# Optimization experiments

Hardware: AMD Instinct MI355X
Metric: run time of the kernel (lower is better)

## Reference

```python
import jax, jax.numpy as jnp
import numpy as np
from itertools import combinations

DIM = 3
METRIC = np.array([1.0, 1.0, 1.0], dtype=np.float32)
KERNEL_SIZE = 7
C_IN, C_OUT = 32, 32
HIDDEN = 64
NUM_LAYERS = 4
N_GRID = KERNEL_SIZE ** DIM


def _build_cayley(dim, metric):
    blades = [()] + [c for r in range(1, dim + 1) for c in combinations(range(dim), r)]
    idx = {b: i for i, b in enumerate(blades)}
    n = len(blades)
    C = np.zeros((n, n, n), dtype=np.float32)
    for i, a in enumerate(blades):
        for j, b in enumerate(blades):
            arr = list(a) + list(b)
            sign = 1.0
            changed = True
            while changed:
                changed = False
                t = 0
                while t < len(arr) - 1:
                    if arr[t] == arr[t + 1]:
                        sign *= metric[arr[t]]
                        del arr[t:t + 2]
                        changed = True
                        break
                    if arr[t] > arr[t + 1]:
                        arr[t], arr[t + 1] = arr[t + 1], arr[t]
                        sign = -sign
                        changed = True
                    t += 1
            C[i, j, idx[tuple(arr)]] = sign
    grades = np.array([len(b) for b in blades])
    return C, grades

_C_LRO, GRADES = _build_cayley(DIM, METRIC)
CAYLEY = np.transpose(_C_LRO, (0, 2, 1))  # [left, out, right] (CEGNN convention)
N_BLADES = CAYLEY.shape[0]
N_GRADES = DIM + 1

# nonzero grade-triple paths of the Cayley tensor and blade-level path-id lookup
_gp = np.zeros((N_GRADES,) * 3, dtype=bool)
for a in range(N_GRADES):
    for b in range(N_GRADES):
        for c in range(N_GRADES):
            _gp[a, b, c] = np.any(CAYLEY[np.ix_(GRADES == a, GRADES == b, GRADES == c)] != 0)
PATHS = np.argwhere(_gp)
P = len(PATHS)
assert P == 20  # product_paths_sum for Cl(3,0)
_pid = -np.ones((N_GRADES,) * 3, dtype=np.int64)
for p, (a, b, c) in enumerate(PATHS):
    _pid[a, b, c] = p
BLADE_PID = _pid[GRADES[:, None, None], GRADES[None, :, None], GRADES[None, None, :]]
BLADE_PID = np.where(BLADE_PID < 0, P, BLADE_PID)  # P -> zero slot

# centered relative-position grid, (N, 1, dim)
_ax = np.arange(KERNEL_SIZE, dtype=np.float32) - (KERNEL_SIZE - 1) / 2.0
_grid = np.stack(np.meshgrid(*([_ax] * DIM), indexing='ij'), axis=-1).reshape(-1, DIM)
REL_POS = jnp.asarray(_grid[:, None, :])
CAYLEY_J = jnp.asarray(CAYLEY)
GRADE_ONEHOT = jnp.asarray((GRADES[:, None] == np.arange(N_GRADES)[None, :]).astype(np.float32))
FACTOR = 1.0 / np.sqrt(float(KERNEL_SIZE ** DIM))
BLADES_OF = {g: np.where(GRADES == g)[0] for g in range(N_GRADES)}


def embed_grade(x, g):
    out = jnp.zeros(x.shape[:-1] + (N_BLADES,), x.dtype)
    return out.at[..., BLADES_OF[g]].set(x)


def expand_paths(w):
    # (..., P) grade-path weights -> (..., B, B, B) blade-level weights
    wz = jnp.concatenate([w, jnp.zeros(w.shape[:-1] + (1,), w.dtype)], axis=-1)
    return wz[..., BLADE_PID]


def mv_linear(x, W, b):
    # grade-wise equivariant channel mixing; x: (N,Ci,B), W: (G,Co,Ci), bias on scalar blade
    y = jnp.einsum('boi,nib->nob', W[GRADES], x)
    return y.at[:, :, 0].add(b)


def mv_silu(x, a, b):
    # gate each grade by sigmoid of its (learned-scaled) squared norm
    qg = jnp.einsum('ncb,bg->ncg', x * x, GRADE_ONEHOT)
    gate = jax.nn.sigmoid(a * qg + b)
    return x * gate[:, :, GRADES]


def gp_layer(x, w):
    # fully-connected steerable geometric product; x: (N,C,B), w: (Co,C,P)
    wc = expand_paths(w) * CAYLEY_J  # (Co, C, B, B, B)
    y = jnp.einsum('nik,oikjm,nim->noj', x, wc, x)
    return y / np.sqrt(float(x.shape[1]))


def setup_inputs() -> dict:
    key = jax.random.key(0)
    ks = jax.random.split(key, 8)
    G, B, H, Pn = N_GRADES, N_BLADES, HIDDEN, P
    rn = lambda k, s, sc: jax.random.normal(k, s, dtype=jnp.float32) * sc
    ci1 = C_IN + 1
    return {
        'condition': rn(ks[0], (C_IN, B), 1.0),
        'rel_pos_sigma': jnp.ones((1, 1, 1), jnp.float32),
        'cayley_w': rn(ks[1], (C_OUT, C_IN, Pn), 1.0 / np.sqrt(C_IN)),
        'lin0_W': rn(ks[2], (G, H, ci1), 1.0 / np.sqrt(ci1)),
        'lin0_b': jnp.zeros((H,), jnp.float32),
        'act0_a': rn(ks[3], (H, G), 0.2),
        'act0_b': jnp.zeros((H, G), jnp.float32),
        'gps_w': rn(ks[4], (NUM_LAYERS, H, H, Pn), 0.5 / np.sqrt(H)),
        'lins_W': rn(ks[5], (NUM_LAYERS - 1, G, H, H), 1.0 / np.sqrt(H)),
        'lins_b': jnp.zeros((NUM_LAYERS - 1, H), jnp.float32),
        'acts_a': rn(ks[6], (NUM_LAYERS - 1, H, G), 0.2),
        'acts_b': jnp.zeros((NUM_LAYERS - 1, H, G), jnp.float32),
        'out_W': rn(ks[7], (G, C_OUT * C_IN, H), 1.0 / np.sqrt(H)),
        'out_b': jnp.zeros((C_OUT * C_IN,), jnp.float32),
        'shell_sigma': jnp.ones((1, C_OUT, C_IN, B), jnp.float32),
    }


def reference(condition, rel_pos_sigma, cayley_w, lin0_W, lin0_b, act0_a, act0_b,
              gps_w, lins_W, lins_b, acts_a, acts_b, out_W, out_b, shell_sigma):
    metric = jnp.asarray(METRIC)
    q = jnp.sum(metric * REL_POS * REL_POS, axis=-1, keepdims=True)  # (N,1,1)
    scalar = jnp.exp(-q / (2.0 * rel_pos_sigma ** 2))
    x = embed_grade(scalar, 0) + embed_grade(REL_POS, 1)  # (N,1,B)
    cond = jnp.broadcast_to(condition[None], (N_GRID,) + condition.shape)
    x = jnp.concatenate([x, cond], axis=1)  # (N, c_in+1, B)
    # kernel network: CEGNN blocks [MVLinear -> MVSiLU -> steerable geometric product]
    h = gp_layer(mv_silu(mv_linear(x, lin0_W, lin0_b), act0_a, act0_b), gps_w[0])
    for l in range(NUM_LAYERS - 1):
        h = gp_layer(mv_silu(mv_linear(h, lins_W[l], lins_b[l]), acts_a[l], acts_b[l]), gps_w[l + 1])
    k = mv_linear(h, out_W, out_b).reshape(N_GRID, C_OUT, C_IN, N_BLADES)
    # per-(c_out,c_in,blade) scalar radial shell
    shell = jnp.exp(-q.reshape(N_GRID, 1, 1, 1) / (shell_sigma ** 2))
    k = k * shell * FACTOR
    # kernel head: sparse weighted-Cayley contraction
    wc = expand_paths(cayley_w) * CAYLEY_J  # (c_out, c_in, B, B, B)
    K = jnp.einsum('noik,oiklm->olimn', k, wc)
    return K.reshape(C_OUT * N_BLADES, C_IN * N_BLADES, KERNEL_SIZE, KERNEL_SIZE, KERNEL_SIZE)
```

## Files before the change

### kernel.cpp

```cpp
#include <hip/hip_runtime.h>
#include <math.h>

#define NB 8
#define NGRID 343
#define HID 64
#define NPATH 20

struct Tab {
  int prod_idx[8][8];
  int prod_sgn[8][8];
  int pid[4][4][4];
  int grade[8];
  int kk_idx[8][8];
  int kk_sgn[8][8];
};

constexpr Tab make_tab() {
  Tab t{};
  int mask[8]  = {0,1,2,4,3,5,6,7};
  int idxof[8] = {0,1,2,4,3,5,6,7};
  for (int k = 0; k < 8; ++k) {
    int g = 0;
    for (int b = 0; b < 3; ++b) g += (mask[k] >> b) & 1;
    t.grade[k] = g;
  }
  for (int k = 0; k < 8; ++k)
    for (int m = 0; m < 8; ++m) {
      int A = mask[k], B = mask[m];
      t.prod_idx[k][m] = idxof[A ^ B];
      int c = 0;
      for (int i = 0; i < 3; ++i)
        if ((B >> i) & 1)
          for (int j = i + 1; j < 3; ++j)
            if ((A >> j) & 1) c++;
      t.prod_sgn[k][m] = (c & 1) ? -1 : 1;
    }
  int pc = 0;
  for (int a = 0; a < 4; ++a)
    for (int b = 0; b < 4; ++b)
      for (int c = 0; c < 4; ++c) {
        bool ok = false;
        for (int k = 0; k < 8; ++k)
          for (int m = 0; m < 8; ++m)
            if (t.grade[k] == a && t.grade[m] == c &&
                t.grade[t.prod_idx[k][m]] == b)
              ok = true;
        t.pid[a][b][c] = ok ? pc++ : NPATH;
      }
  for (int l = 0; l < 8; ++l)
    for (int m = 0; m < 8; ++m)
      for (int k = 0; k < 8; ++k)
        if (t.prod_idx[k][m] == l) {
          t.kk_idx[l][m] = k;
          t.kk_sgn[l][m] = t.prod_sgn[k][m];
        }
  return t;
}
constexpr Tab TB = make_tab();

#define OFF_LIN0T 0
#define OFF_LINST 8448
#define OFF_GPST  57600
#define OFF_OUTWT 385280
#define OFF_KWS   647424

__global__ void ccs_prep_kernel(const float* __restrict__ lin0_W,
                                const float* __restrict__ lins_W,
                                const float* __restrict__ gps_w,
                                const float* __restrict__ out_W,
                                float* __restrict__ ws) {
  const int TOT = 8448 + 49152 + 327680 + 262144;
  for (int d = blockIdx.x * blockDim.x + threadIdx.x; d < TOT;
       d += gridDim.x * blockDim.x) {
    float v;
    if (d < 8448) {
      int idx = d;
      int hh = idx & 63, ch = (idx >> 6) % 33, g = (idx >> 6) / 33;
      v = lin0_W[(g * 64 + hh) * 33 + ch];
    } else if (d < 8448 + 49152) {
      int idx = d - OFF_LINST;
      int hh = idx & 63, i = (idx >> 6) & 63, g = (idx >> 12) & 3, l = idx >> 14;
      v = lins_W[((l * 4 + g) * 64 + hh) * 64 + i];
    } else if (d < 8448 + 49152 + 327680) {
      int idx = d - OFF_GPST;
      int o = idx & 63, p = (idx >> 6) % 20, i = ((idx >> 6) / 20) & 63,
          l = idx / 81920;
      v = gps_w[((l * 64 + o) * 64 + i) * 20 + p];
    } else {
      int idx = d - OFF_OUTWT;
      int oc = idx & 1023, i = (idx >> 10) & 63, g = idx >> 16;
      v = out_W[(g * 1024 + oc) * 64 + i];
    }
    ws[d] = v;
  }
}

__launch_bounds__(512)
__global__ void ccs_net_kernel(const float* __restrict__ condition,
                               const float* __restrict__ rel_pos_sigma,
                               const float* __restrict__ lin0_b,
                               const float* __restrict__ act0_a,
                               const float* __restrict__ act0_b,
                               const float* __restrict__ lins_b,
                               const float* __restrict__ acts_a,
                               const float* __restrict__ acts_b,
                               const float* __restrict__ out_b,
                               const float* __restrict__ shell_sigma,
                               const float* __restrict__ ws,
                               float* __restrict__ kws) {
  const float* lin0t = ws + OFF_LIN0T;
  const float* linst = ws + OFF_LINST;
  const float* gpst  = ws + OFF_GPST;
  const float* outwt = ws + OFF_OUTWT;

  __shared__ float xb[33 * 8];
  __shared__ float x0r[2][8];
  __shared__ __align__(16) float F0[2 * 512];
  __shared__ __align__(16) float F1[2 * 512];
  __shared__ float part[2 * 8 * 8 * 64];

  const int tid = threadIdx.x;
  const int n0 = blockIdx.x * 2;
  const int n1 = n0 + 1;

  const float sig = rel_pos_sigma[0];

  float qq[2];
  {
    int iz = n0 % 7, iy = (n0 / 7) % 7, ix = n0 / 49;
    float px = (float)ix - 3.f, py = (float)iy - 3.f, pz = (float)iz - 3.f;
    qq[0] = px * px + py * py + pz * pz;
  }
  {
    int nc = (n1 < NGRID) ? n1 : (NGRID - 1);
    int iz = nc % 7, iy = (nc / 7) % 7, ix = nc / 49;
    float px = (float)ix - 3.f, py = (float)iy - 3.f, pz = (float)iz - 3.f;
    qq[1] = px * px + py * py + pz * pz;
  }

  for (int t = tid; t < 264; t += 512) {
    int ch = t >> 3, b = t & 7;
    xb[t] = (ch == 0) ? 0.f : condition[(ch - 1) * 8 + b];
  }
  if (tid < 16) {
    int pt = tid >> 3, b = tid & 7;
    int nc = n0 + pt;
    if (nc >= NGRID) nc = NGRID - 1;
    int iz = nc % 7, iy = (nc / 7) % 7, ix = nc / 49;
    float px = (float)ix - 3.f, py = (float)iy - 3.f, pz = (float)iz - 3.f;
    float q = px * px + py * py + pz * pz;
    float scal = expf(-q / (2.f * sig * sig));
    x0r[pt][b] =
        (b == 0) ? scal : (b == 1) ? px : (b == 2) ? py : (b == 3) ? pz : 0.f;
  }
  __syncthreads();

  const int b8 = tid & 7;
  const int hh = (tid >> 3) & 63;
  const int gb = TB.grade[b8];

  {
    const float* wrow = lin0t + gb * 33 * 64 + hh;
    float w0 = wrow[0];
    float a0 = w0 * x0r[0][b8];
    float a1 = w0 * x0r[1][b8];
    if (b8 == 0) {
      float bb = lin0_b[hh];
      a0 += bb;
      a1 += bb;
    }
    #pragma unroll
    for (int ch = 1; ch < 33; ++ch) {
      float w = wrow[ch * 64];
      float xv = xb[ch * 8 + b8];
      a0 = fmaf(w, xv, a0);
      a1 = fmaf(w, xv, a1);
    }
    F0[hh * 8 + b8] = a0;
    F0[512 + hh * 8 + b8] = a1;
  }
  __syncthreads();

  auto silu = [&](const float* src, float* dst, const float* aa,
                  const float* bb) {
    int s0 = (gb == 0) ? 0 : (gb == 1) ? 1 : (gb == 2) ? 4 : 7;
    int cnt = (gb == 0 || gb == 3) ? 1 : 3;
    float A = aa[hh * 4 + gb], B = bb[hh * 4 + gb];
    #pragma unroll
    for (int pt = 0; pt < 2; ++pt) {
      float qg = 0.f;
      for (int u = 0; u < cnt; ++u) {
        float v = src[pt * 512 + hh * 8 + s0 + u];
        qg = fmaf(v, v, qg);
      }
      float z = fmaf(A, qg, B);
      float gate = 1.f / (1.f + expf(-z));
      dst[pt * 512 + hh * 8 + b8] = src[pt * 512 + hh * 8 + b8] * gate;
    }
  };

  auto lin = [&](const float* src, float* dst, const float* wt,
                 const float* bias) {
    const float* wrow = wt + gb * 64 * 64 + hh;
    float a0 = 0.f, a1 = 0.f;
    if (b8 == 0) {
      float bb = bias[hh];
      a0 = bb;
      a1 = bb;
    }
    #pragma unroll
    for (int i = 0; i < 64; ++i) {
      float w = wrow[i * 64];
      a0 = fmaf(w, src[i * 8 + b8], a0);
      a1 = fmaf(w, src[512 + i * 8 + b8], a1);
    }
    dst[hh * 8 + b8] = a0;
    dst[512 + hh * 8 + b8] = a1;
  };

  auto gp = [&](const float* src, float* dst, const float* wl) {
    const int o = tid & 63;
    const int isub = tid >> 6;
    float fa[8], fb[8];
    #pragma unroll
    for (int j = 0; j < 8; ++j) {
      fa[j] = 0.f;
      fb[j] = 0.f;
    }
    for (int it = 0; it < 8; ++it) {
      int i = isub * 8 + it;
      float4 va0 = *(const float4*)(src + i * 8);
      float4 va1 = *(const float4*)(src + i * 8 + 4);
      float4 vb0 = *(const float4*)(src + 512 + i * 8);
      float4 vb1 = *(const float4*)(src + 512 + i * 8 + 4);
      float xA[8] = {va0.x, va0.y, va0.z, va0.w, va1.x, va1.y, va1.z, va1.w};
      float xB[8] = {vb0.x, vb0.y, vb0.z, vb0.w, vb1.x, vb1.y, vb1.z, vb1.w};
      const float* wb = wl + i * 20 * 64 + o;
      float wp[20];
      #pragma unroll
      for (int p = 0; p < 20; ++p) wp[p] = wb[p * 64];
      #pragma unroll
      for (int k = 0; k < 8; ++k) {
        #pragma unroll
        for (int m = 0; m < 8; ++m) {
          const int j = TB.prod_idx[k][m];
          const int p = TB.pid[TB.grade[k]][TB.grade[j]][TB.grade[m]];
          if (TB.prod_sgn[k][m] > 0) {
            fa[j] = fmaf(xA[k] * xA[m], wp[p], fa[j]);
            fb[j] = fmaf(xB[k] * xB[m], wp[p], fb[j]);
          } else {
            fa[j] = fmaf(-xA[k] * xA[m], wp[p], fa[j]);
            fb[j] = fmaf(-xB[k] * xB[m], wp[p], fb[j]);
          }
        }
      }
    }
    #pragma unroll
    for (int j = 0; j < 8; ++j) {
      part[isub * 512 + j * 64 + o] = fa[j];
      part[4096 + isub * 512 + j * 64 + o] = fb[j];
    }
    __syncthreads();
    #pragma unroll
    for (int r = 0; r < 2; ++r) {
      int item = tid + r * 512;
      int oo = item & 63;
      int j = (item >> 6) & 7;
      int pt = item >> 9;
      const float* pp = part + pt * 4096 + j * 64 + oo;
      float s = pp[0] + pp[512] + pp[1024] + pp[1536] + pp[2048] + pp[2560] +
                pp[3072] + pp[3584];
      dst[pt * 512 + oo * 8 + j] = s * 0.125f;
    }
    __syncthreads();
  };

  silu(F0, F1, act0_a, act0_b);
  __syncthreads();
  gp(F1, F0, gpst + 0);

  float* f = F0;
  float* g_ = F1;
  for (int l = 0; l < 3; ++l) {
    lin(f, g_, linst + l * 16384, lins_b + l * 64);
    __syncthreads();
    silu(g_, f, acts_a + l * 256, acts_b + l * 256);
    __syncthreads();
    gp(f, g_, gpst + (l + 1) * 81920);
    float* t = f; f = g_; g_ = t;
  }

  const float FACTOR = 1.0f / sqrtf(343.0f);
  #pragma unroll
  for (int r = 0; r < 2; ++r) {
    int oc = tid + r * 512;
    float acc[2][8];
    #pragma unroll
    for (int pt = 0; pt < 2; ++pt)
      #pragma unroll
      for (int b = 0; b < 8; ++b) acc[pt][b] = 0.f;
    {
      float bb = out_b[oc];
      acc[0][0] = bb;
      acc[1][0] = bb;
    }
    #pragma unroll 4
    for (int i = 0; i < 64; ++i) {
      float w0 = outwt[(0 * 64 + i) * 1024 + oc];
      float w1 = outwt[(1 * 64 + i) * 1024 + oc];
      float w2 = outwt[(2 * 64 + i) * 1024 + oc];
      float w3 = outwt[(3 * 64 + i) * 1024 + oc];
      #pragma unroll
      for (int pt = 0; pt < 2; ++pt) {
        float h[8];
        *(float4*)h = *(const float4*)(f + pt * 512 + i * 8);
        *(float4*)(h + 4) = *(const float4*)(f + pt * 512 + i * 8 + 4);
        acc[pt][0] = fmaf(w0, h[0], acc[pt][0]);
        acc[pt][1] = fmaf(w1, h[1], acc[pt][1]);
        acc[pt][2] = fmaf(w1, h[2], acc[pt][2]);
        acc[pt][3] = fmaf(w1, h[3], acc[pt][3]);
        acc[pt][4] = fmaf(w2, h[4], acc[pt][4]);
        acc[pt][5] = fmaf(w2, h[5], acc[pt][5]);
        acc[pt][6] = fmaf(w2, h[6], acc[pt][6]);
        acc[pt][7] = fmaf(w3, h[7], acc[pt][7]);
      }
    }
    float sh[8];
    *(float4*)sh = *(const float4*)(shell_sigma + oc * 8);
    *(float4*)(sh + 4) = *(const float4*)(shell_sigma + oc * 8 + 4);
    #pragma unroll
    for (int pt = 0; pt < 2; ++pt) {
      int n = n0 + pt;
      if (n < NGRID) {
        float q = qq[pt];
        float out8[8];
        #pragma unroll
        for (int b = 0; b < 8; ++b)
          out8[b] = acc[pt][b] * expf(-q / (sh[b] * sh[b])) * FACTOR;
        float4* dstp = (float4*)(kws + ((size_t)oc * 343 + n) * 8);
        dstp[0] = make_float4(out8[0], out8[1], out8[2], out8[3]);
        dstp[1] = make_float4(out8[4], out8[5], out8[6], out8[7]);
      }
    }
  }
}

__launch_bounds__(256)
__global__ void ccs_expand_kernel(const float* __restrict__ cayley_w,
                                  const float* __restrict__ kws,
                                  float* __restrict__ out) {
  const int oi = blockIdx.x;
  const int tid = threadIdx.x;
  __shared__ float kT[8][344];

  const float4* src = (const float4*)(kws + (size_t)oi * 343 * 8);
  for (int t = tid; t < 686; t += 256) {
    float4 v = src[t];
    int n = t >> 1, b = (t & 1) * 4;
    kT[b][n] = v.x;
    kT[b + 1][n] = v.y;
    kT[b + 2][n] = v.z;
    kT[b + 3][n] = v.w;
  }
  float cw[20];
  #pragma unroll
  for (int p = 0; p < 20; ++p) cw[p] = cayley_w[oi * 20 + p];
  __syncthreads();

  const int o = oi >> 5, i = oi & 31;
  #pragma unroll
  for (int l = 0; l < 8; ++l) {
    #pragma unroll
    for (int m = 0; m < 8; ++m) {
      const int kk = TB.kk_idx[l][m];
      const int p = TB.pid[TB.grade[kk]][TB.grade[l]][TB.grade[m]];
      float c = (TB.kk_sgn[l][m] < 0) ? -cw[p] : cw[p];
      float* dst = out + ((size_t)((o * 8 + l) * 256 + i * 8 + m)) * 343;
      dst[tid] = kT[kk][tid] * c;
      if (tid < 343 - 256) dst[tid + 256] = kT[kk][tid + 256] * c;
    }
  }
}

extern "C" void kernel_launch(void* const* d_in, const int* in_sizes, int n_in,
                              void* d_out, int out_size, void* d_ws,
                              size_t ws_size, hipStream_t stream) {
  const float* condition     = (const float*)d_in[0];
  const float* rel_pos_sigma = (const float*)d_in[1];
  const float* cayley_w      = (const float*)d_in[2];
  const float* lin0_W        = (const float*)d_in[3];
  const float* lin0_b        = (const float*)d_in[4];
  const float* act0_a        = (const float*)d_in[5];
  const float* act0_b        = (const float*)d_in[6];
  const float* gps_w         = (const float*)d_in[7];
  const float* lins_W        = (const float*)d_in[8];
  const float* lins_b        = (const float*)d_in[9];
  const float* acts_a        = (const float*)d_in[10];
  const float* acts_b        = (const float*)d_in[11];
  const float* out_W         = (const float*)d_in[12];
  const float* out_b         = (const float*)d_in[13];
  const float* shell_sigma   = (const float*)d_in[14];

  float* ws = (float*)d_ws;
  float* kws = ws + OFF_KWS;
  float* out = (float*)d_out;

  ccs_prep_kernel<<<dim3(640), dim3(256), 0, stream>>>(lin0_W, lins_W, gps_w,
                                                       out_W, ws);
  ccs_net_kernel<<<dim3((NGRID + 1) / 2), dim3(512), 0, stream>>>(
      condition, rel_pos_sigma, lin0_b, act0_a, act0_b, lins_b, acts_a, acts_b,
      out_b, shell_sigma, ws, kws);
  ccs_expand_kernel<<<dim3(1024), dim3(256), 0, stream>>>(cayley_w, kws, out);
}
```

Measured before the change: 226.2 us.

## Double-buffer geometric-product weights into LDS with async global_load_lds prefetch

The geometric-product layer now streams its per-layer weights into a two-slot LDS buffer using asynchronous global-to-LDS loads, issued two chunks ahead. Explicit vmcnt waits replace the per-iteration global loads. The input-channel mapping is changed so each wave consumes only the chunk slice it loaded itself, which avoids block barriers. The goal is to hide global-memory latency behind the FMA-heavy product loop. In exchange it adds about 80 KB of LDS per block and relies on hand-counted vmcnt values, which is fragile if the compiler emits other vector-memory operations.

```diff
diff --git a/kernel.cpp b/kernel.cpp
--- a/kernel.cpp
+++ b/kernel.cpp
@@ -95,6 +95,12 @@
   }
 }
 
+__device__ __forceinline__ void glds16(const float* g, float* l) {
+  __builtin_amdgcn_global_load_lds(
+      (const __attribute__((address_space(1))) unsigned int*)g,
+      (__attribute__((address_space(3))) unsigned int*)l, 16, 0, 0);
+}
+
 __launch_bounds__(512)
 __global__ void ccs_net_kernel(const float* __restrict__ condition,
                                const float* __restrict__ rel_pos_sigma,
@@ -118,6 +124,7 @@
   __shared__ __align__(16) float F0[2 * 512];
   __shared__ __align__(16) float F1[2 * 512];
   __shared__ float part[2 * 8 * 8 * 64];
+  __shared__ __align__(16) float wch[2][10240];
 
   const int tid = threadIdx.x;
   const int n0 = blockIdx.x * 2;
@@ -220,25 +227,43 @@
 
   auto gp = [&](const float* src, float* dst, const float* wl) {
     const int o = tid & 63;
-    const int isub = tid >> 6;
+    const int w = tid >> 6;
+    const int w5 = w * 5;
+    const int ln4 = (tid & 63) * 4;
     float fa[8], fb[8];
     #pragma unroll
     for (int j = 0; j < 8; ++j) {
       fa[j] = 0.f;
       fb[j] = 0.f;
     }
-    for (int it = 0; it < 8; ++it) {
-      int i = isub * 8 + it;
+    auto issue = [&](int c) {
+      const float* gbch = wl + c * 10240;
+      float* lbch = &wch[c & 1][0];
+      #pragma unroll
+      for (int u = 0; u < 5; ++u) {
+        int t = w5 + u;
+        glds16(gbch + t * 256 + ln4, lbch + t * 256);
+      }
+    };
+    issue(0);
+    issue(1);
+    for (int c = 0; c < 8; ++c) {
+      if (c < 7) {
+        asm volatile("s_waitcnt vmcnt(5)" ::: "memory");
+      } else {
+        asm volatile("s_waitcnt vmcnt(0)" ::: "memory");
+      }
+      const int i = c * 8 + w;
+      const float* wp_l = &wch[c & 1][w * 1280 + o];
+      float wp[20];
+      #pragma unroll
+      for (int p = 0; p < 20; ++p) wp[p] = wp_l[p * 64];
       float4 va0 = *(const float4*)(src + i * 8);
       float4 va1 = *(const float4*)(src + i * 8 + 4);
       float4 vb0 = *(const float4*)(src + 512 + i * 8);
       float4 vb1 = *(const float4*)(src + 512 + i * 8 + 4);
       float xA[8] = {va0.x, va0.y, va0.z, va0.w, va1.x, va1.y, va1.z, va1.w};
       float xB[8] = {vb0.x, vb0.y, vb0.z, vb0.w, vb1.x, vb1.y, vb1.z, vb1.w};
-      const float* wb = wl + i * 20 * 64 + o;
-      float wp[20];
-      #pragma unroll
-      for (int p = 0; p < 20; ++p) wp[p] = wb[p * 64];
       #pragma unroll
       for (int k = 0; k < 8; ++k) {
         #pragma unroll
@@ -254,11 +279,12 @@
           }
         }
       }
+      if (c < 6) issue(c + 2);
     }
     #pragma unroll
     for (int j = 0; j < 8; ++j) {
-      part[isub * 512 + j * 64 + o] = fa[j];
-      part[4096 + isub * 512 + j * 64 + o] = fb[j];
+      part[w * 512 + j * 64 + o] = fa[j];
+      part[4096 + w * 512 + j * 64 + o] = fb[j];
     }
     __syncthreads();
     #pragma unroll
```

New measurement: 223.4 us. About the same (-1.2%).
